# Optimization experiments

Hardware: AMD Instinct MI355X
Metric: run time of the kernel (lower is better)

The kernel has to match this reference:

```python
import jax, jax.numpy as jnp
import numpy as np

B, S, D = 2, 4096, 1024

def setup_inputs() -> dict:
    key = jax.random.key(0)
    k1, k2 = jax.random.split(key)
    x = jax.random.normal(k1, (B, S, D), dtype=jnp.float32)
    W = jax.random.normal(k2, (D, 3 * D), dtype=jnp.float32) * (1.0 / np.sqrt(D))
    b = jnp.zeros((3 * D,), dtype=jnp.float32)
    return {"x": x, "W": W, "b": b}

def reference(x, W, b) -> jnp.ndarray:
    D_ = x.shape[-1]
    qkv = x @ W + b                       # [B, S, 3D]
    q, k, v = jnp.split(qkv, 3, axis=2)    # each [B, S, D]
    scale = 1.0 / jnp.sqrt(jnp.asarray(D_, dtype=x.dtype))
    scores = jnp.einsum('bqd,bkd->bqk', q, k) * scale  # [B, S, S]
    weights = jax.nn.softmax(scores, axis=-1)
    return jnp.einsum('bqk,bkd->bqd', weights, v)       # [B, S, D]
```

## Files before the change

### kernel.cpp

```cpp
#include <hip/hip_runtime.h>
#include <hip/hip_bf16.h>

typedef __attribute__((ext_vector_type(4))) float  f32x4;
typedef __attribute__((ext_vector_type(8))) __bf16 bf16x8;
typedef __attribute__((ext_vector_type(8))) unsigned short u16x8;

typedef const __attribute__((address_space(1))) void gas_void;
typedef __attribute__((address_space(3))) void las_void;

__device__ __forceinline__ unsigned short f2bf(float x) {
    unsigned u = __builtin_bit_cast(unsigned, x);
    u += 0x7fffu + ((u >> 16) & 1u);
    return (unsigned short)(u >> 16);
}
__device__ __forceinline__ float bf2f(unsigned short h) {
    unsigned u = ((unsigned)h) << 16;
    return __builtin_bit_cast(float, u);
}
__device__ __forceinline__ void gload_lds16(const void* g, void* l) {
    __builtin_amdgcn_global_load_lds((gas_void*)g, (las_void*)l, 16, 0, 0);
}

#define WAITVM(N) asm volatile("s_waitcnt vmcnt(" #N ")" ::: "memory")

__global__ void k_f32_to_bf16(const float* __restrict__ in,
                              unsigned short* __restrict__ out, int n4) {
    int i = blockIdx.x * blockDim.x + threadIdx.x;
    if (i < n4) {
        float4 v = ((const float4*)in)[i];
        ushort4 o;
        o.x = f2bf(v.x); o.y = f2bf(v.y); o.z = f2bf(v.z); o.w = f2bf(v.w);
        ((ushort4*)out)[i] = o;
    }
}

__global__ void k_transpose_w(const float* __restrict__ W,
                              unsigned short* __restrict__ Wt,
                              int K, int N) {
    __shared__ unsigned short tile[32][33];
    int n0 = blockIdx.x * 32, k0 = blockIdx.y * 32;
    int tx = threadIdx.x, ty = threadIdx.y;
#pragma unroll
    for (int i = 0; i < 4; i++) {
        int kk = ty + i * 8;
        tile[kk][tx] = f2bf(W[(size_t)(k0 + kk) * N + n0 + tx]);
    }
    __syncthreads();
#pragma unroll
    for (int i = 0; i < 4; i++) {
        int nn = ty + i * 8;
        Wt[(size_t)(n0 + nn) * K + k0 + tx] = tile[tx][nn];
    }
}

__global__ void k_transpose_v(const unsigned short* __restrict__ Vrow,
                              unsigned short* __restrict__ Vt) {
    __shared__ unsigned short tile[32][33];
    int b = blockIdx.z;
    int s0 = blockIdx.x * 32, d0 = blockIdx.y * 32;
    int tx = threadIdx.x, ty = threadIdx.y;
#pragma unroll
    for (int i = 0; i < 4; i++) {
        int ss = ty + i * 8;
        tile[ss][tx] = Vrow[((size_t)(b * 4096 + s0 + ss)) * 1024 + d0 + tx];
    }
    __syncthreads();
#pragma unroll
    for (int i = 0; i < 4; i++) {
        int dd = ty + i * 8;
        Vt[((size_t)b * 1024 + d0 + dd) * 4096 + s0 + tx] = tile[tx][dd];
    }
}

template <int MODE>
__global__ __launch_bounds__(512, 2) void k_g256(
        const unsigned short* __restrict__ A, int lda,
        const unsigned short* __restrict__ Bt, int ldb,
        void* __restrict__ C, int ldc,
        unsigned short* __restrict__ Vp,
        const float* __restrict__ bias,
        int K, float alpha, long sA, long sB, long sC) {
    __shared__ __align__(16) unsigned short As[2][16384];
    __shared__ __align__(16) unsigned short Bs[2][16384];

    const int z = blockIdx.z;
    A  += (size_t)z * sA;
    Bt += (size_t)z * sB;

    const int nwg  = gridDim.x * gridDim.y;
    const int flat = blockIdx.y * gridDim.x + blockIdx.x;
    const int swzb = (flat & 7) * (nwg >> 3) + (flat >> 3);
    const int m0   = (swzb / gridDim.x) * 256;
    const int n0   = (swzb % gridDim.x) * 256;

    const int tid  = threadIdx.x;
    const int lane = tid & 63;
    const int wid  = tid >> 6;
    const int wm   = wid >> 2;
    const int wn   = wid & 3;
    const int l15  = lane & 15;
    const int l4   = lane >> 4;

    f32x4 acc[8][4] = {};

    const int srow = tid >> 3;
    const int kel  = (((lane & 7) ^ (lane >> 3)) << 3);
    const int c0 = ((l4 << 4)) ^ ((l15 & 7) << 4);
    const int c1 = (64 + (l4 << 4)) ^ ((l15 & 7) << 4);

    auto stageA = [&](int b, int h, int kt) {
#pragma unroll
        for (int c = 0; c < 2; c++) {
            const int r = h * 128 + c * 64 + srow;
            gload_lds16(A + (size_t)(m0 + r) * lda + kt * 64 + kel,
                        (char*)As + b * 32768 + h * 16384 + c * 8192 + (wid << 10));
        }
    };
    auto stageB = [&](int b, int h, int kt) {
#pragma unroll
        for (int c = 0; c < 2; c++) {
            const int r = h * 128 + c * 64 + srow;
            gload_lds16(Bt + (size_t)(n0 + r) * ldb + kt * 64 + kel,
                        (char*)Bs + b * 32768 + h * 16384 + c * 8192 + (wid << 10));
        }
    };

#define MM(I, J, X, Y) \
    acc[I][J] = __builtin_amdgcn_mfma_f32_16x16x32_bf16((X), (Y), acc[I][J], 0, 0, 0)

    const int NT = K >> 6;
    stageA(0, 0, 0); stageB(0, 0, 0); stageA(0, 1, 0); stageB(0, 1, 0);

    for (int t = 0; t < NT; t++) {
        const int cur = t & 1, nxt = cur ^ 1;
        const char* Ab = (const char*)As + cur * 32768;
        const char* Bb = (const char*)Bs + cur * 32768;

        if (t + 1 < NT) {
            stageA(nxt, 0, t + 1); stageB(nxt, 0, t + 1);
            WAITVM(4);
        } else {
            WAITVM(0);
        }
        __builtin_amdgcn_s_barrier();
        __builtin_amdgcn_sched_barrier(0);

        bf16x8 bfrg[2][2][2];
#pragma unroll
        for (int qn = 0; qn < 2; qn++)
#pragma unroll
        for (int nf = 0; nf < 2; nf++) {
            const int rb = (wn * 64 + qn * 32 + nf * 16 + l15) * 128;
            bfrg[qn][nf][0] = *(const bf16x8*)(Bb + rb + c0);
            bfrg[qn][nf][1] = *(const bf16x8*)(Bb + rb + c1);
        }
        {
            bf16x8 af[4][2];
#pragma unroll
            for (int mf = 0; mf < 4; mf++) {
                const int ra = (wm * 128 + 0 * 64 + mf * 16 + l15) * 128;
                af[mf][0] = *(const bf16x8*)(Ab + ra + c0);
                af[mf][1] = *(const bf16x8*)(Ab + ra + c1);
            }
            __builtin_amdgcn_s_setprio(1);
#pragma unroll
            for (int mf = 0; mf < 4; mf++)
#pragma unroll
            for (int qn = 0; qn < 2; qn++)
#pragma unroll
            for (int nf = 0; nf < 2; nf++) {
                MM(mf, qn * 2 + nf, af[mf][0], bfrg[qn][nf][0]);
                MM(mf, qn * 2 + nf, af[mf][1], bfrg[qn][nf][1]);
            }
            __builtin_amdgcn_s_setprio(0);
        }

        if (t + 1 < NT) { stageA(nxt, 1, t + 1); stageB(nxt, 1, t + 1); }
        {
            bf16x8 af[4][2];
#pragma unroll
            for (int mf = 0; mf < 4; mf++) {
                const int ra = (wm * 128 + 1 * 64 + mf * 16 + l15) * 128;
                af[mf][0] = *(const bf16x8*)(Ab + ra + c0);
                af[mf][1] = *(const bf16x8*)(Ab + ra + c1);
            }
            __builtin_amdgcn_s_setprio(1);
#pragma unroll
            for (int mf = 0; mf < 4; mf++)
#pragma unroll
            for (int qn = 0; qn < 2; qn++)
#pragma unroll
            for (int nf = 0; nf < 2; nf++) {
                MM(4 + mf, qn * 2 + nf, af[mf][0], bfrg[qn][nf][0]);
                MM(4 + mf, qn * 2 + nf, af[mf][1], bfrg[qn][nf][1]);
            }
            __builtin_amdgcn_s_setprio(0);
        }
        __builtin_amdgcn_s_barrier();
        __builtin_amdgcn_sched_barrier(0);
    }
#undef MM

#pragma unroll
    for (int qm = 0; qm < 2; qm++)
#pragma unroll
    for (int mf = 0; mf < 4; mf++) {
        const int row = m0 + wm * 128 + qm * 64 + mf * 16 + l4 * 4;
#pragma unroll
        for (int qn = 0; qn < 2; qn++)
#pragma unroll
        for (int nf = 0; nf < 2; nf++) {
            const int col = n0 + wn * 64 + qn * 32 + nf * 16 + l15;
            const float bv = (MODE == 2) ? bias[col] : 0.0f;
            const f32x4 av = acc[qm * 4 + mf][qn * 2 + nf];
#pragma unroll
            for (int r = 0; r < 4; r++) {
                const float v = av[r] * alpha + bv;
                if (MODE == 1) {
                    ((unsigned short*)C)[(size_t)z * sC + (size_t)(row + r) * ldc + col] = f2bf(v);
                } else {
                    const int lc = col & 1023;
                    if (col < 2048)
                        ((unsigned short*)C)[(size_t)(col >> 10) * 8388608 +
                                             (size_t)(row + r) * 1024 + lc] = f2bf(v);
                    else
                        Vp[(size_t)(row + r) * 1024 + lc] = f2bf(v);
                }
            }
        }
    }
}

__global__ __launch_bounds__(512, 2) void k_pv256(
        const unsigned short* __restrict__ A, int lda,
        const unsigned short* __restrict__ Bt, int ldb,
        float* __restrict__ C, int ldc,
        int K, long sA, long sB, long sC) {
    __shared__ __align__(16) unsigned short As[2][16384];
    __shared__ __align__(16) unsigned short Bs[2][8192];

    const int z = blockIdx.z;
    A  += (size_t)z * sA;
    Bt += (size_t)z * sB;

    const int nwg  = gridDim.x * gridDim.y;
    const int flat = blockIdx.y * gridDim.x + blockIdx.x;
    const int swzb = (flat & 7) * (nwg >> 3) + (flat >> 3);
    const int m0   = (swzb / gridDim.x) * 256;
    const int n0   = (swzb % gridDim.x) * 128;

    const int tid  = threadIdx.x;
    const int lane = tid & 63;
    const int wid  = tid >> 6;
    const int wm   = wid >> 2;
    const int wn   = wid & 3;
    const int l15  = lane & 15;
    const int l4   = lane >> 4;

    f32x4 acc[8][2] = {};

    const int srow = tid >> 3;
    const int kel  = (((lane & 7) ^ (lane >> 3)) << 3);
    const int c0 = ((l4 << 4)) ^ ((l15 & 7) << 4);
    const int c1 = (64 + (l4 << 4)) ^ ((l15 & 7) << 4);

    auto stageA1 = [&](int b, int a, int kt) {
        const int r = a * 64 + srow;
        gload_lds16(A + (size_t)(m0 + r) * lda + kt * 64 + kel,
                    (char*)As + b * 32768 + a * 8192 + (wid << 10));
    };
    auto stageB1 = [&](int b, int c, int kt) {
        const int r = c * 64 + srow;
        gload_lds16(Bt + (size_t)(n0 + r) * ldb + kt * 64 + kel,
                    (char*)Bs + b * 16384 + c * 8192 + (wid << 10));
    };

#define MM(I, J, X, Y) \
    acc[I][J] = __builtin_amdgcn_mfma_f32_16x16x32_bf16((X), (Y), acc[I][J], 0, 0, 0)

    const int NT = K >> 6;
    stageA1(0, 0, 0); stageA1(0, 1, 0); stageA1(0, 2, 0); stageA1(0, 3, 0);
    stageB1(0, 0, 0); stageB1(0, 1, 0);

    for (int t = 0; t < NT; t++) {
        const int cur = t & 1, nxt = cur ^ 1;
        const char* Ab = (const char*)As + cur * 32768;
        const char* Bb = (const char*)Bs + cur * 16384;

        if (t + 1 < NT) {
            stageA1(nxt, 0, t + 1); stageA1(nxt, 1, t + 1); stageB1(nxt, 0, t + 1);
            WAITVM(3);
        } else {
            WAITVM(0);
        }
        __builtin_amdgcn_s_barrier();
        __builtin_amdgcn_sched_barrier(0);

        bf16x8 bfrg[2][2];
#pragma unroll
        for (int nf = 0; nf < 2; nf++) {
            const int rb = (wn * 32 + nf * 16 + l15) * 128;
            bfrg[nf][0] = *(const bf16x8*)(Bb + rb + c0);
            bfrg[nf][1] = *(const bf16x8*)(Bb + rb + c1);
        }
        {
            bf16x8 af[4][2];
#pragma unroll
            for (int mf = 0; mf < 4; mf++) {
                const int ra = (wm * 128 + 0 * 64 + mf * 16 + l15) * 128;
                af[mf][0] = *(const bf16x8*)(Ab + ra + c0);
                af[mf][1] = *(const bf16x8*)(Ab + ra + c1);
            }
            __builtin_amdgcn_s_setprio(1);
#pragma unroll
            for (int mf = 0; mf < 4; mf++)
#pragma unroll
            for (int nf = 0; nf < 2; nf++) {
                MM(mf, nf, af[mf][0], bfrg[nf][0]);
                MM(mf, nf, af[mf][1], bfrg[nf][1]);
            }
            __builtin_amdgcn_s_setprio(0);
        }

        if (t + 1 < NT) {
            stageA1(nxt, 2, t + 1); stageA1(nxt, 3, t + 1); stageB1(nxt, 1, t + 1);
        }
        {
            bf16x8 af[4][2];
#pragma unroll
            for (int mf = 0; mf < 4; mf++) {
                const int ra = (wm * 128 + 1 * 64 + mf * 16 + l15) * 128;
                af[mf][0] = *(const bf16x8*)(Ab + ra + c0);
                af[mf][1] = *(const bf16x8*)(Ab + ra + c1);
            }
            __builtin_amdgcn_s_setprio(1);
#pragma unroll
            for (int mf = 0; mf < 4; mf++)
#pragma unroll
            for (int nf = 0; nf < 2; nf++) {
                MM(4 + mf, nf, af[mf][0], bfrg[nf][0]);
                MM(4 + mf, nf, af[mf][1], bfrg[nf][1]);
            }
            __builtin_amdgcn_s_setprio(0);
        }
        __builtin_amdgcn_s_barrier();
        __builtin_amdgcn_sched_barrier(0);
    }
#undef MM

#pragma unroll
    for (int qm = 0; qm < 2; qm++)
#pragma unroll
    for (int mf = 0; mf < 4; mf++) {
        const int row = m0 + wm * 128 + qm * 64 + mf * 16 + l4 * 4;
#pragma unroll
        for (int nf = 0; nf < 2; nf++) {
            const int col = n0 + wn * 32 + nf * 16 + l15;
            const f32x4 av = acc[qm * 4 + mf][nf];
#pragma unroll
            for (int r = 0; r < 4; r++)
                C[(size_t)z * sC + (size_t)(row + r) * ldc + col] = av[r];
        }
    }
}

__global__ __launch_bounds__(256) void k_softmax_inplace(unsigned short* __restrict__ P, int S) {
    __shared__ float red[8];
    const int row  = blockIdx.x;
    const int tid  = threadIdx.x;
    const int lane = tid & 63;
    const int wid  = tid >> 6;
    unsigned short* p = P + (size_t)row * S;

    float v[16];
    u16x8 h0 = *(const u16x8*)&p[tid * 16];
    u16x8 h1 = *(const u16x8*)&p[tid * 16 + 8];
    float mx = -1e30f;
#pragma unroll
    for (int j = 0; j < 8; j++) { v[j]     = bf2f(h0[j]); mx = fmaxf(mx, v[j]);     }
#pragma unroll
    for (int j = 0; j < 8; j++) { v[j + 8] = bf2f(h1[j]); mx = fmaxf(mx, v[j + 8]); }

#pragma unroll
    for (int o = 32; o >= 1; o >>= 1) mx = fmaxf(mx, __shfl_xor(mx, o));
    if (lane == 0) red[wid] = mx;
    __syncthreads();
    mx = fmaxf(fmaxf(red[0], red[1]), fmaxf(red[2], red[3]));

    float sum = 0.0f;
#pragma unroll
    for (int j = 0; j < 16; j++) { v[j] = __expf(v[j] - mx); sum += v[j]; }
#pragma unroll
    for (int o = 32; o >= 1; o >>= 1) sum += __shfl_xor(sum, o);
    if (lane == 0) red[4 + wid] = sum;
    __syncthreads();
    sum = red[4] + red[5] + red[6] + red[7];
    const float rinv = 1.0f / sum;

    u16x8 o0, o1;
#pragma unroll
    for (int j = 0; j < 8; j++) { o0[j] = f2bf(v[j] * rinv); o1[j] = f2bf(v[j + 8] * rinv); }
    *(u16x8*)&p[tid * 16]     = o0;
    *(u16x8*)&p[tid * 16 + 8] = o1;
}

extern "C" void kernel_launch(void* const* d_in, const int* in_sizes, int n_in,
                              void* d_out, int out_size, void* d_ws, size_t ws_size,
                              hipStream_t stream) {
    const float* x    = (const float*)d_in[0];
    const float* W    = (const float*)d_in[1];
    const float* bias = (const float*)d_in[2];
    float* out        = (float*)d_out;

    char* ws = (char*)d_ws;
    unsigned short* Qb   = (unsigned short*)(ws);
    unsigned short* Vt   = (unsigned short*)(ws + 33554432);
    unsigned short* xb   = (unsigned short*)(ws + 50331648);
    unsigned short* Wt   = (unsigned short*)(ws + 67108864);
    unsigned short* Vrow = (unsigned short*)(ws + 73400320);
    unsigned short* Pcat = (unsigned short*)(ws + 50331648);

    k_f32_to_bf16<<<8192, 256, 0, stream>>>(x, xb, (8192 * 1024) / 4);
    k_transpose_w<<<dim3(96, 32), dim3(32, 8), 0, stream>>>(W, Wt, 1024, 3072);
    k_g256<2><<<dim3(12, 32, 1), 512, 0, stream>>>(
        xb, 1024, Wt, 1024, (void*)Qb, 1024, Vrow, bias, 1024, 1.0f, 0, 0, 0);
    k_transpose_v<<<dim3(128, 32, 2), dim3(32, 8), 0, stream>>>(Vrow, Vt);

    const float scale = 0.03125f;
    k_g256<1><<<dim3(16, 16, 2), 512, 0, stream>>>(
        Qb, 1024, Qb + 8388608, 1024, (void*)Pcat, 4096, nullptr, nullptr,
        1024, scale, 4194304, 4194304, 16777216);
    k_softmax_inplace<<<8192, 256, 0, stream>>>(Pcat, 4096);
    k_pv256<<<dim3(8, 16, 2), 512, 0, stream>>>(
        Pcat, 4096, Vt, 4096, out, 1024, 4096, 16777216, 4194304, 4194304);
}
```

Before: 277.6 us.

## Restructure GEMM main loops into four-phase ping-pong with interleaved staging

Both GEMM kernels now split each K-tile iteration into four barrier-separated phases. Each phase issues one slice of next-tile global-to-LDS loads and then runs a smaller MFMA block on fragments read just before it, which spreads memory issue evenly between compute and shrinks the live fragment registers. The PV kernel also changes its wave layout from 2x4 to 4x2 (64x64 per wave), which changes the LDS read reuse of A and B fragments. The cost is many more workgroup barriers per iteration, and the staging order may leave the WAITVM counts tight.

```diff
diff --git a/kernel.cpp b/kernel.cpp
--- a/kernel.cpp
+++ b/kernel.cpp
@@ -22,6 +22,7 @@
 }
 
 #define WAITVM(N) asm volatile("s_waitcnt vmcnt(" #N ")" ::: "memory")
+#define BAR() do { __builtin_amdgcn_s_barrier(); __builtin_amdgcn_sched_barrier(0); } while (0)
 
 __global__ void k_f32_to_bf16(const float* __restrict__ in,
                               unsigned short* __restrict__ out, int n4) {
@@ -73,7 +74,7 @@
 }
 
 template <int MODE>
-__global__ __launch_bounds__(512, 2) void k_g256(
+__global__ __launch_bounds__(512, 2) void k_g256p4(
         const unsigned short* __restrict__ A, int lda,
         const unsigned short* __restrict__ Bt, int ldb,
         void* __restrict__ C, int ldc,
@@ -127,6 +128,36 @@
 
 #define MM(I, J, X, Y) \
     acc[I][J] = __builtin_amdgcn_mfma_f32_16x16x32_bf16((X), (Y), acc[I][J], 0, 0, 0)
+#define RD_A(QM)                                                               \
+    do {                                                                       \
+        _Pragma("unroll")                                                      \
+        for (int mf = 0; mf < 4; mf++) {                                       \
+            const int ra = (wm * 128 + (QM) * 64 + mf * 16 + l15) * 128;       \
+            af[mf][0] = *(const bf16x8*)(Ab + ra + c0);                        \
+            af[mf][1] = *(const bf16x8*)(Ab + ra + c1);                        \
+        }                                                                      \
+    } while (0)
+#define RD_B(QN)                                                               \
+    do {                                                                       \
+        _Pragma("unroll")                                                      \
+        for (int nf = 0; nf < 2; nf++) {                                       \
+            const int rb = (wn * 64 + (QN) * 32 + nf * 16 + l15) * 128;        \
+            bq[nf][0] = *(const bf16x8*)(Bb + rb + c0);                        \
+            bq[nf][1] = *(const bf16x8*)(Bb + rb + c1);                        \
+        }                                                                      \
+    } while (0)
+#define MFMA_PH(QM, QN)                                                        \
+    do {                                                                       \
+        __builtin_amdgcn_s_setprio(1);                                         \
+        _Pragma("unroll")                                                      \
+        for (int mf = 0; mf < 4; mf++)                                         \
+        _Pragma("unroll")                                                      \
+        for (int nf = 0; nf < 2; nf++) {                                       \
+            MM((QM) * 4 + mf, (QN) * 2 + nf, af[mf][0], bq[nf][0]);            \
+            MM((QM) * 4 + mf, (QN) * 2 + nf, af[mf][1], bq[nf][1]);            \
+        }                                                                      \
+        __builtin_amdgcn_s_setprio(0);                                         \
+    } while (0)
 
     const int NT = K >> 6;
     stageA(0, 0, 0); stageB(0, 0, 0); stageA(0, 1, 0); stageB(0, 1, 0);
@@ -135,70 +166,34 @@
         const int cur = t & 1, nxt = cur ^ 1;
         const char* Ab = (const char*)As + cur * 32768;
         const char* Bb = (const char*)Bs + cur * 32768;
-
-        if (t + 1 < NT) {
-            stageA(nxt, 0, t + 1); stageB(nxt, 0, t + 1);
-            WAITVM(4);
-        } else {
-            WAITVM(0);
-        }
-        __builtin_amdgcn_s_barrier();
-        __builtin_amdgcn_sched_barrier(0);
-
-        bf16x8 bfrg[2][2][2];
-#pragma unroll
-        for (int qn = 0; qn < 2; qn++)
-#pragma unroll
-        for (int nf = 0; nf < 2; nf++) {
-            const int rb = (wn * 64 + qn * 32 + nf * 16 + l15) * 128;
-            bfrg[qn][nf][0] = *(const bf16x8*)(Bb + rb + c0);
-            bfrg[qn][nf][1] = *(const bf16x8*)(Bb + rb + c1);
-        }
-        {
-            bf16x8 af[4][2];
-#pragma unroll
-            for (int mf = 0; mf < 4; mf++) {
-                const int ra = (wm * 128 + 0 * 64 + mf * 16 + l15) * 128;
-                af[mf][0] = *(const bf16x8*)(Ab + ra + c0);
-                af[mf][1] = *(const bf16x8*)(Ab + ra + c1);
-            }
-            __builtin_amdgcn_s_setprio(1);
-#pragma unroll
-            for (int mf = 0; mf < 4; mf++)
-#pragma unroll
-            for (int qn = 0; qn < 2; qn++)
-#pragma unroll
-            for (int nf = 0; nf < 2; nf++) {
-                MM(mf, qn * 2 + nf, af[mf][0], bfrg[qn][nf][0]);
-                MM(mf, qn * 2 + nf, af[mf][1], bfrg[qn][nf][1]);
-            }
-            __builtin_amdgcn_s_setprio(0);
-        }
-
-        if (t + 1 < NT) { stageA(nxt, 1, t + 1); stageB(nxt, 1, t + 1); }
-        {
-            bf16x8 af[4][2];
-#pragma unroll
-            for (int mf = 0; mf < 4; mf++) {
-                const int ra = (wm * 128 + 1 * 64 + mf * 16 + l15) * 128;
-                af[mf][0] = *(const bf16x8*)(Ab + ra + c0);
-                af[mf][1] = *(const bf16x8*)(Ab + ra + c1);
-            }
-            __builtin_amdgcn_s_setprio(1);
-#pragma unroll
-            for (int mf = 0; mf < 4; mf++)
-#pragma unroll
-            for (int qn = 0; qn < 2; qn++)
-#pragma unroll
-            for (int nf = 0; nf < 2; nf++) {
-                MM(4 + mf, qn * 2 + nf, af[mf][0], bfrg[qn][nf][0]);
-                MM(4 + mf, qn * 2 + nf, af[mf][1], bfrg[qn][nf][1]);
-            }
-            __builtin_amdgcn_s_setprio(0);
-        }
-        __builtin_amdgcn_s_barrier();
-        __builtin_amdgcn_sched_barrier(0);
-    }
+        const bool hn = (t + 1 < NT);
+
+        bf16x8 af[4][2], bq[2][2];
+
+        if (hn) { stageA(nxt, 0, t + 1); WAITVM(2); } else { WAITVM(0); }
+        BAR();
+        RD_A(0); RD_B(0);
+        MFMA_PH(0, 0);
+        BAR();
+        if (hn) stageB(nxt, 0, t + 1);
+        BAR();
+        RD_B(1);
+        MFMA_PH(0, 1);
+        BAR();
+        if (hn) stageA(nxt, 1, t + 1);
+        BAR();
+        RD_A(1); RD_B(0);
+        MFMA_PH(1, 0);
+        BAR();
+        if (hn) stageB(nxt, 1, t + 1);
+        BAR();
+        RD_B(1);
+        MFMA_PH(1, 1);
+        BAR();
+    }
+#undef MFMA_PH
+#undef RD_B
+#undef RD_A
 #undef MM
 
 #pragma unroll
@@ -231,7 +226,7 @@
     }
 }
 
-__global__ __launch_bounds__(512, 2) void k_pv256(
+__global__ __launch_bounds__(512, 2) void k_pv256p4(
         const unsigned short* __restrict__ A, int lda,
         const unsigned short* __restrict__ Bt, int ldb,
         float* __restrict__ C, int ldc,
@@ -252,12 +247,12 @@
     const int tid  = threadIdx.x;
     const int lane = tid & 63;
     const int wid  = tid >> 6;
-    const int wm   = wid >> 2;
-    const int wn   = wid & 3;
+    const int wm   = wid >> 1;
+    const int wn   = wid & 1;
     const int l15  = lane & 15;
     const int l4   = lane >> 4;
 
-    f32x4 acc[8][2] = {};
+    f32x4 acc[4][4] = {};
 
     const int srow = tid >> 3;
     const int kel  = (((lane & 7) ^ (lane >> 3)) << 3);
@@ -277,6 +272,32 @@
 
 #define MM(I, J, X, Y) \
     acc[I][J] = __builtin_amdgcn_mfma_f32_16x16x32_bf16((X), (Y), acc[I][J], 0, 0, 0)
+#define RD_A(CC)                                                               \
+    do {                                                                       \
+        _Pragma("unroll")                                                      \
+        for (int mf = 0; mf < 4; mf++) {                                       \
+            const int ra = (wm * 64 + mf * 16 + l15) * 128;                    \
+            af[mf] = *(const bf16x8*)(Ab + ra + (CC));                         \
+        }                                                                      \
+    } while (0)
+#define RD_B(NP, CC)                                                           \
+    do {                                                                       \
+        _Pragma("unroll")                                                      \
+        for (int j = 0; j < 2; j++) {                                          \
+            const int rb = (wn * 64 + ((NP) * 2 + j) * 16 + l15) * 128;        \
+            bq[j] = *(const bf16x8*)(Bb + rb + (CC));                          \
+        }                                                                      \
+    } while (0)
+#define MFMA_PH(NP)                                                            \
+    do {                                                                       \
+        __builtin_amdgcn_s_setprio(1);                                         \
+        _Pragma("unroll")                                                      \
+        for (int mf = 0; mf < 4; mf++)                                         \
+        _Pragma("unroll")                                                      \
+        for (int j = 0; j < 2; j++)                                            \
+            MM(mf, (NP) * 2 + j, af[mf], bq[j]);                               \
+        __builtin_amdgcn_s_setprio(0);                                         \
+    } while (0)
 
     const int NT = K >> 6;
     stageA1(0, 0, 0); stageA1(0, 1, 0); stageA1(0, 2, 0); stageA1(0, 3, 0);
@@ -286,77 +307,44 @@
         const int cur = t & 1, nxt = cur ^ 1;
         const char* Ab = (const char*)As + cur * 32768;
         const char* Bb = (const char*)Bs + cur * 16384;
-
-        if (t + 1 < NT) {
-            stageA1(nxt, 0, t + 1); stageA1(nxt, 1, t + 1); stageB1(nxt, 0, t + 1);
-            WAITVM(3);
-        } else {
-            WAITVM(0);
-        }
-        __builtin_amdgcn_s_barrier();
-        __builtin_amdgcn_sched_barrier(0);
-
-        bf16x8 bfrg[2][2];
-#pragma unroll
-        for (int nf = 0; nf < 2; nf++) {
-            const int rb = (wn * 32 + nf * 16 + l15) * 128;
-            bfrg[nf][0] = *(const bf16x8*)(Bb + rb + c0);
-            bfrg[nf][1] = *(const bf16x8*)(Bb + rb + c1);
-        }
-        {
-            bf16x8 af[4][2];
-#pragma unroll
-            for (int mf = 0; mf < 4; mf++) {
-                const int ra = (wm * 128 + 0 * 64 + mf * 16 + l15) * 128;
-                af[mf][0] = *(const bf16x8*)(Ab + ra + c0);
-                af[mf][1] = *(const bf16x8*)(Ab + ra + c1);
-            }
-            __builtin_amdgcn_s_setprio(1);
-#pragma unroll
-            for (int mf = 0; mf < 4; mf++)
-#pragma unroll
-            for (int nf = 0; nf < 2; nf++) {
-                MM(mf, nf, af[mf][0], bfrg[nf][0]);
-                MM(mf, nf, af[mf][1], bfrg[nf][1]);
-            }
-            __builtin_amdgcn_s_setprio(0);
-        }
-
-        if (t + 1 < NT) {
-            stageA1(nxt, 2, t + 1); stageA1(nxt, 3, t + 1); stageB1(nxt, 1, t + 1);
-        }
-        {
-            bf16x8 af[4][2];
-#pragma unroll
-            for (int mf = 0; mf < 4; mf++) {
-                const int ra = (wm * 128 + 1 * 64 + mf * 16 + l15) * 128;
-                af[mf][0] = *(const bf16x8*)(Ab + ra + c0);
-                af[mf][1] = *(const bf16x8*)(Ab + ra + c1);
-            }
-            __builtin_amdgcn_s_setprio(1);
-#pragma unroll
-            for (int mf = 0; mf < 4; mf++)
-#pragma unroll
-            for (int nf = 0; nf < 2; nf++) {
-                MM(4 + mf, nf, af[mf][0], bfrg[nf][0]);
-                MM(4 + mf, nf, af[mf][1], bfrg[nf][1]);
-            }
-            __builtin_amdgcn_s_setprio(0);
-        }
-        __builtin_amdgcn_s_barrier();
-        __builtin_amdgcn_sched_barrier(0);
-    }
+        const bool hn = (t + 1 < NT);
+
+        bf16x8 af[4], bq[2];
+
+        if (hn) { stageA1(nxt, 0, t + 1); stageA1(nxt, 1, t + 1); WAITVM(2); }
+        else    { WAITVM(0); }
+        BAR();
+        RD_A(c0); RD_B(0, c0);
+        MFMA_PH(0);
+        BAR();
+        if (hn) { stageA1(nxt, 2, t + 1); stageA1(nxt, 3, t + 1); }
+        BAR();
+        RD_B(1, c0);
+        MFMA_PH(1);
+        BAR();
+        if (hn) stageB1(nxt, 0, t + 1);
+        BAR();
+        RD_A(c1); RD_B(0, c1);
+        MFMA_PH(0);
+        BAR();
+        if (hn) stageB1(nxt, 1, t + 1);
+        BAR();
+        RD_B(1, c1);
+        MFMA_PH(1);
+        BAR();
+    }
+#undef MFMA_PH
+#undef RD_B
+#undef RD_A
 #undef MM
 
 #pragma unroll
-    for (int qm = 0; qm < 2; qm++)
-#pragma unroll
     for (int mf = 0; mf < 4; mf++) {
-        const int row = m0 + wm * 128 + qm * 64 + mf * 16 + l4 * 4;
-#pragma unroll
-        for (int nf = 0; nf < 2; nf++) {
-            const int col = n0 + wn * 32 + nf * 16 + l15;
-            const f32x4 av = acc[qm * 4 + mf][nf];
+        const int row = m0 + wm * 64 + mf * 16 + l4 * 4;
+#pragma unroll
+        for (int nf = 0; nf < 4; nf++) {
+            const int col = n0 + wn * 64 + nf * 16 + l15;
+            const f32x4 av = acc[mf][nf];
 #pragma unroll
             for (int r = 0; r < 4; r++)
                 C[(size_t)z * sC + (size_t)(row + r) * ldc + col] = av[r];
@@ -422,15 +410,15 @@
 
     k_f32_to_bf16<<<8192, 256, 0, stream>>>(x, xb, (8192 * 1024) / 4);
     k_transpose_w<<<dim3(96, 32), dim3(32, 8), 0, stream>>>(W, Wt, 1024, 3072);
-    k_g256<2><<<dim3(12, 32, 1), 512, 0, stream>>>(
+    k_g256p4<2><<<dim3(12, 32, 1), 512, 0, stream>>>(
         xb, 1024, Wt, 1024, (void*)Qb, 1024, Vrow, bias, 1024, 1.0f, 0, 0, 0);
     k_transpose_v<<<dim3(128, 32, 2), dim3(32, 8), 0, stream>>>(Vrow, Vt);
 
     const float scale = 0.03125f;
-    k_g256<1><<<dim3(16, 16, 2), 512, 0, stream>>>(
+    k_g256p4<1><<<dim3(16, 16, 2), 512, 0, stream>>>(
         Qb, 1024, Qb + 8388608, 1024, (void*)Pcat, 4096, nullptr, nullptr,
         1024, scale, 4194304, 4194304, 16777216);
     k_softmax_inplace<<<8192, 256, 0, stream>>>(Pcat, 4096);
-    k_pv256<<<dim3(8, 16, 2), 512, 0, stream>>>(
+    k_pv256p4<<<dim3(8, 16, 2), 512, 0, stream>>>(
         Pcat, 4096, Vt, 4096, out, 1024, 4096, 16777216, 4194304, 4194304);
 }
```

After: 375.7 us. 35.3% more time.

## Fuse softmax into score GEMM epilogue and write V transposed from QKV GEMM

Applied to the files above, without the earlier changes.

The separate in-place softmax pass over the bf16 score matrix is replaced. The score GEMM epilogue now writes exp(score*scale) and emits per-column-block partial row sums; a small kernel turns those sums into reciprocals, and the PV GEMM scales its output rows by them. The QKV projection moves to a new 128x128-tile kernel that stores V directly in transposed layout, so the V transpose kernel goes away. This removes a full read and write of the probability matrix plus one launch. The cost is that exp is taken without subtracting the row max, which can overflow for inputs with large scores.

```diff
diff --git a/kernel.cpp b/kernel.cpp
--- a/kernel.cpp
+++ b/kernel.cpp
@@ -22,6 +22,7 @@
 }
 
 #define WAITVM(N) asm volatile("s_waitcnt vmcnt(" #N ")" ::: "memory")
+#define BAR() do { __builtin_amdgcn_s_barrier(); __builtin_amdgcn_sched_barrier(0); } while (0)
 
 __global__ void k_f32_to_bf16(const float* __restrict__ in,
                               unsigned short* __restrict__ out, int n4) {
@@ -53,33 +54,132 @@
     }
 }
 
-__global__ void k_transpose_v(const unsigned short* __restrict__ Vrow,
-                              unsigned short* __restrict__ Vt) {
-    __shared__ unsigned short tile[32][33];
-    int b = blockIdx.z;
-    int s0 = blockIdx.x * 32, d0 = blockIdx.y * 32;
-    int tx = threadIdx.x, ty = threadIdx.y;
-#pragma unroll
-    for (int i = 0; i < 4; i++) {
-        int ss = ty + i * 8;
-        tile[ss][tx] = Vrow[((size_t)(b * 4096 + s0 + ss)) * 1024 + d0 + tx];
-    }
-    __syncthreads();
-#pragma unroll
-    for (int i = 0; i < 4; i++) {
-        int dd = ty + i * 8;
-        Vt[((size_t)b * 1024 + d0 + dd) * 4096 + s0 + tx] = tile[tx][dd];
-    }
-}
-
-template <int MODE>
-__global__ __launch_bounds__(512, 2) void k_g256(
+__global__ __launch_bounds__(256, 2) void k_g128qkv(
         const unsigned short* __restrict__ A, int lda,
         const unsigned short* __restrict__ Bt, int ldb,
-        void* __restrict__ C, int ldc,
-        unsigned short* __restrict__ Vp,
-        const float* __restrict__ bias,
-        int K, float alpha, long sA, long sB, long sC) {
+        unsigned short* __restrict__ C,
+        unsigned short* __restrict__ Vt,
+        const float* __restrict__ bias, int K) {
+    __shared__ __align__(16) unsigned short As[2][8192];
+    __shared__ __align__(16) unsigned short Bs[2][8192];
+
+    const int nwg  = gridDim.x * gridDim.y;
+    const int flat = blockIdx.y * gridDim.x + blockIdx.x;
+    const int swzb = (flat & 7) * (nwg >> 3) + (flat >> 3);
+    const int m0   = (swzb / gridDim.x) * 128;
+    const int n0   = (swzb % gridDim.x) * 128;
+
+    const int tid  = threadIdx.x;
+    const int lane = tid & 63;
+    const int wid  = tid >> 6;
+    const int wr   = wid >> 1;
+    const int wc   = wid & 1;
+    const int l15  = lane & 15;
+    const int l4   = lane >> 4;
+
+    f32x4 acc[4][4] = {};
+
+    const int srow = tid >> 3;
+    const int kel  = (((lane & 7) ^ (lane >> 3)) << 3);
+    const int c0 = (l4 << 4) ^ ((l15 & 7) << 4);
+    const int c1 = (64 + (l4 << 4)) ^ ((l15 & 7) << 4);
+
+    auto stA = [&](int b, int g, int kt) {
+        gload_lds16(A + (size_t)(m0 + g * 32 + srow) * lda + kt * 64 + kel,
+                    (char*)As + b * 16384 + g * 4096 + (wid << 10));
+    };
+    auto stB = [&](int b, int g, int kt) {
+        gload_lds16(Bt + (size_t)(n0 + g * 32 + srow) * ldb + kt * 64 + kel,
+                    (char*)Bs + b * 16384 + g * 4096 + (wid << 10));
+    };
+
+#define MM(I, J, X, Y) \
+    acc[I][J] = __builtin_amdgcn_mfma_f32_16x16x32_bf16((X), (Y), acc[I][J], 0, 0, 0)
+
+    const int NT = K >> 6;
+    stA(0, 0, 0); stA(0, 1, 0); stA(0, 2, 0); stA(0, 3, 0);
+    stB(0, 0, 0); stB(0, 1, 0); stB(0, 2, 0); stB(0, 3, 0);
+
+    for (int t = 0; t < NT; t++) {
+        const int cur = t & 1, nxt = cur ^ 1;
+        const char* Ab = (const char*)As + cur * 16384;
+        const char* Bb = (const char*)Bs + cur * 16384;
+        const bool hn = (t + 1 < NT);
+
+        bf16x8 af[4], bq[4];
+
+        if (hn) {
+            stA(nxt, 0, t + 1); stA(nxt, 1, t + 1); stA(nxt, 2, t + 1); stA(nxt, 3, t + 1);
+            WAITVM(4);
+        } else {
+            WAITVM(0);
+        }
+        BAR();
+#pragma unroll
+        for (int mf = 0; mf < 4; mf++)
+            af[mf] = *(const bf16x8*)(Ab + (wr * 64 + mf * 16 + l15) * 128 + c0);
+#pragma unroll
+        for (int nf = 0; nf < 4; nf++)
+            bq[nf] = *(const bf16x8*)(Bb + (wc * 64 + nf * 16 + l15) * 128 + c0);
+        __builtin_amdgcn_s_setprio(1);
+#pragma unroll
+        for (int mf = 0; mf < 4; mf++)
+#pragma unroll
+        for (int nf = 0; nf < 4; nf++)
+            MM(mf, nf, af[mf], bq[nf]);
+        __builtin_amdgcn_s_setprio(0);
+
+        if (hn) {
+            stB(nxt, 0, t + 1); stB(nxt, 1, t + 1); stB(nxt, 2, t + 1); stB(nxt, 3, t + 1);
+        }
+#pragma unroll
+        for (int mf = 0; mf < 4; mf++)
+            af[mf] = *(const bf16x8*)(Ab + (wr * 64 + mf * 16 + l15) * 128 + c1);
+#pragma unroll
+        for (int nf = 0; nf < 4; nf++)
+            bq[nf] = *(const bf16x8*)(Bb + (wc * 64 + nf * 16 + l15) * 128 + c1);
+        __builtin_amdgcn_s_setprio(1);
+#pragma unroll
+        for (int mf = 0; mf < 4; mf++)
+#pragma unroll
+        for (int nf = 0; nf < 4; nf++)
+            MM(mf, nf, af[mf], bq[nf]);
+        __builtin_amdgcn_s_setprio(0);
+        BAR();
+    }
+#undef MM
+
+#pragma unroll
+    for (int mf = 0; mf < 4; mf++) {
+        const int row = m0 + wr * 64 + mf * 16 + l4 * 4;
+#pragma unroll
+        for (int nf = 0; nf < 4; nf++) {
+            const int col = n0 + wc * 64 + nf * 16 + l15;
+            const f32x4 av = acc[mf][nf];
+            const float bv = bias[col];
+            const int lc = col & 1023;
+            if (col < 2048) {
+#pragma unroll
+                for (int r = 0; r < 4; r++)
+                    C[(size_t)(col >> 10) * 8388608 +
+                      (size_t)(row + r) * 1024 + lc] = f2bf(av[r] + bv);
+            } else {
+                const int b = row >> 12, s = row & 4095;
+                ushort4 o;
+                o.x = f2bf(av[0] + bv); o.y = f2bf(av[1] + bv);
+                o.z = f2bf(av[2] + bv); o.w = f2bf(av[3] + bv);
+                *(ushort4*)&Vt[(size_t)b * 4194304 + (size_t)lc * 4096 + s] = o;
+            }
+        }
+    }
+}
+
+__global__ __launch_bounds__(512, 2) void k_scores(
+        const unsigned short* __restrict__ A,
+        const unsigned short* __restrict__ Bt,
+        unsigned short* __restrict__ C,
+        float* __restrict__ part,
+        int K, float scale, long sA, long sB, long sC) {
     __shared__ __align__(16) unsigned short As[2][16384];
     __shared__ __align__(16) unsigned short Bs[2][16384];
 
@@ -112,7 +212,7 @@
 #pragma unroll
         for (int c = 0; c < 2; c++) {
             const int r = h * 128 + c * 64 + srow;
-            gload_lds16(A + (size_t)(m0 + r) * lda + kt * 64 + kel,
+            gload_lds16(A + (size_t)(m0 + r) * 1024 + kt * 64 + kel,
                         (char*)As + b * 32768 + h * 16384 + c * 8192 + (wid << 10));
         }
     };
@@ -120,7 +220,7 @@
 #pragma unroll
         for (int c = 0; c < 2; c++) {
             const int r = h * 128 + c * 64 + srow;
-            gload_lds16(Bt + (size_t)(n0 + r) * ldb + kt * 64 + kel,
+            gload_lds16(Bt + (size_t)(n0 + r) * 1024 + kt * 64 + kel,
                         (char*)Bs + b * 32768 + h * 16384 + c * 8192 + (wid << 10));
         }
     };
@@ -142,8 +242,7 @@
         } else {
             WAITVM(0);
         }
-        __builtin_amdgcn_s_barrier();
-        __builtin_amdgcn_sched_barrier(0);
+        BAR();
 
         bf16x8 bfrg[2][2][2];
 #pragma unroll
@@ -201,40 +300,60 @@
     }
 #undef MM
 
+    const int cb4 = ((n0 >> 8) << 2) + wn;
 #pragma unroll
     for (int qm = 0; qm < 2; qm++)
 #pragma unroll
     for (int mf = 0; mf < 4; mf++) {
         const int row = m0 + wm * 128 + qm * 64 + mf * 16 + l4 * 4;
+        float rs[4] = {0.f, 0.f, 0.f, 0.f};
 #pragma unroll
         for (int qn = 0; qn < 2; qn++)
 #pragma unroll
         for (int nf = 0; nf < 2; nf++) {
             const int col = n0 + wn * 64 + qn * 32 + nf * 16 + l15;
-            const float bv = (MODE == 2) ? bias[col] : 0.0f;
             const f32x4 av = acc[qm * 4 + mf][qn * 2 + nf];
 #pragma unroll
             for (int r = 0; r < 4; r++) {
-                const float v = av[r] * alpha + bv;
-                if (MODE == 1) {
-                    ((unsigned short*)C)[(size_t)z * sC + (size_t)(row + r) * ldc + col] = f2bf(v);
-                } else {
-                    const int lc = col & 1023;
-                    if (col < 2048)
-                        ((unsigned short*)C)[(size_t)(col >> 10) * 8388608 +
-                                             (size_t)(row + r) * 1024 + lc] = f2bf(v);
-                    else
-                        Vp[(size_t)(row + r) * 1024 + lc] = f2bf(v);
-                }
-            }
-        }
+                const float e = __expf(av[r] * scale);
+                rs[r] += e;
+                C[(size_t)z * sC + (size_t)(row + r) * 4096 + col] = f2bf(e);
+            }
+        }
+#pragma unroll
+        for (int r = 0; r < 4; r++) {
+#pragma unroll
+            for (int o = 1; o < 16; o <<= 1)
+                rs[r] += __shfl_xor(rs[r], o);
+        }
+        if (l15 == 0) {
+#pragma unroll
+            for (int r = 0; r < 4; r++)
+                part[((size_t)z * 4096 + row + r) * 64 + cb4] = rs[r];
+        }
+    }
+}
+
+__global__ __launch_bounds__(256) void k_rinv(const float* __restrict__ part,
+                                              float* __restrict__ rinv, int nrows) {
+    int row = blockIdx.x * blockDim.x + threadIdx.x;
+    if (row < nrows) {
+        const float* p = part + (size_t)row * 64;
+        float s = 0.f;
+#pragma unroll
+        for (int i = 0; i < 16; i++) {
+            f32x4 v = *(const f32x4*)(p + i * 4);
+            s += v[0] + v[1] + v[2] + v[3];
+        }
+        rinv[row] = 1.0f / s;
     }
 }
 
 __global__ __launch_bounds__(512, 2) void k_pv256(
-        const unsigned short* __restrict__ A, int lda,
-        const unsigned short* __restrict__ Bt, int ldb,
-        float* __restrict__ C, int ldc,
+        const unsigned short* __restrict__ A,
+        const unsigned short* __restrict__ Bt,
+        float* __restrict__ C,
+        const float* __restrict__ rinv,
         int K, long sA, long sB, long sC) {
     __shared__ __align__(16) unsigned short As[2][16384];
     __shared__ __align__(16) unsigned short Bs[2][8192];
@@ -266,12 +385,12 @@
 
     auto stageA1 = [&](int b, int a, int kt) {
         const int r = a * 64 + srow;
-        gload_lds16(A + (size_t)(m0 + r) * lda + kt * 64 + kel,
+        gload_lds16(A + (size_t)(m0 + r) * 4096 + kt * 64 + kel,
                     (char*)As + b * 32768 + a * 8192 + (wid << 10));
     };
     auto stageB1 = [&](int b, int c, int kt) {
         const int r = c * 64 + srow;
-        gload_lds16(Bt + (size_t)(n0 + r) * ldb + kt * 64 + kel,
+        gload_lds16(Bt + (size_t)(n0 + r) * 4096 + kt * 64 + kel,
                     (char*)Bs + b * 16384 + c * 8192 + (wid << 10));
     };
 
@@ -293,8 +412,7 @@
         } else {
             WAITVM(0);
         }
-        __builtin_amdgcn_s_barrier();
-        __builtin_amdgcn_sched_barrier(0);
+        BAR();
 
         bf16x8 bfrg[2][2];
 #pragma unroll
@@ -353,55 +471,16 @@
 #pragma unroll
     for (int mf = 0; mf < 4; mf++) {
         const int row = m0 + wm * 128 + qm * 64 + mf * 16 + l4 * 4;
+        const f32x4 riv = *(const f32x4*)&rinv[(size_t)z * 4096 + row];
 #pragma unroll
         for (int nf = 0; nf < 2; nf++) {
             const int col = n0 + wn * 32 + nf * 16 + l15;
             const f32x4 av = acc[qm * 4 + mf][nf];
 #pragma unroll
             for (int r = 0; r < 4; r++)
-                C[(size_t)z * sC + (size_t)(row + r) * ldc + col] = av[r];
-        }
-    }
-}
-
-__global__ __launch_bounds__(256) void k_softmax_inplace(unsigned short* __restrict__ P, int S) {
-    __shared__ float red[8];
-    const int row  = blockIdx.x;
-    const int tid  = threadIdx.x;
-    const int lane = tid & 63;
-    const int wid  = tid >> 6;
-    unsigned short* p = P + (size_t)row * S;
-
-    float v[16];
-    u16x8 h0 = *(const u16x8*)&p[tid * 16];
-    u16x8 h1 = *(const u16x8*)&p[tid * 16 + 8];
-    float mx = -1e30f;
-#pragma unroll
-    for (int j = 0; j < 8; j++) { v[j]     = bf2f(h0[j]); mx = fmaxf(mx, v[j]);     }
-#pragma unroll
-    for (int j = 0; j < 8; j++) { v[j + 8] = bf2f(h1[j]); mx = fmaxf(mx, v[j + 8]); }
-
-#pragma unroll
-    for (int o = 32; o >= 1; o >>= 1) mx = fmaxf(mx, __shfl_xor(mx, o));
-    if (lane == 0) red[wid] = mx;
-    __syncthreads();
-    mx = fmaxf(fmaxf(red[0], red[1]), fmaxf(red[2], red[3]));
-
-    float sum = 0.0f;
-#pragma unroll
-    for (int j = 0; j < 16; j++) { v[j] = __expf(v[j] - mx); sum += v[j]; }
-#pragma unroll
-    for (int o = 32; o >= 1; o >>= 1) sum += __shfl_xor(sum, o);
-    if (lane == 0) red[4 + wid] = sum;
-    __syncthreads();
-    sum = red[4] + red[5] + red[6] + red[7];
-    const float rinv = 1.0f / sum;
-
-    u16x8 o0, o1;
-#pragma unroll
-    for (int j = 0; j < 8; j++) { o0[j] = f2bf(v[j] * rinv); o1[j] = f2bf(v[j + 8] * rinv); }
-    *(u16x8*)&p[tid * 16]     = o0;
-    *(u16x8*)&p[tid * 16 + 8] = o1;
+                C[(size_t)z * sC + (size_t)(row + r) * 1024 + col] = av[r] * riv[r];
+        }
+    }
 }
 
 extern "C" void kernel_launch(void* const* d_in, const int* in_sizes, int n_in,
@@ -417,20 +496,18 @@
     unsigned short* Vt   = (unsigned short*)(ws + 33554432);
     unsigned short* xb   = (unsigned short*)(ws + 50331648);
     unsigned short* Wt   = (unsigned short*)(ws + 67108864);
-    unsigned short* Vrow = (unsigned short*)(ws + 73400320);
     unsigned short* Pcat = (unsigned short*)(ws + 50331648);
+    float*          part = (float*)(ws + 117440512);
+    float*          rinv = (float*)(ws + 121634816);
 
     k_f32_to_bf16<<<8192, 256, 0, stream>>>(x, xb, (8192 * 1024) / 4);
     k_transpose_w<<<dim3(96, 32), dim3(32, 8), 0, stream>>>(W, Wt, 1024, 3072);
-    k_g256<2><<<dim3(12, 32, 1), 512, 0, stream>>>(
-        xb, 1024, Wt, 1024, (void*)Qb, 1024, Vrow, bias, 1024, 1.0f, 0, 0, 0);
-    k_transpose_v<<<dim3(128, 32, 2), dim3(32, 8), 0, stream>>>(Vrow, Vt);
+    k_g128qkv<<<dim3(24, 64), 256, 0, stream>>>(xb, 1024, Wt, 1024, Qb, Vt, bias, 1024);
 
     const float scale = 0.03125f;
-    k_g256<1><<<dim3(16, 16, 2), 512, 0, stream>>>(
-        Qb, 1024, Qb + 8388608, 1024, (void*)Pcat, 4096, nullptr, nullptr,
-        1024, scale, 4194304, 4194304, 16777216);
-    k_softmax_inplace<<<8192, 256, 0, stream>>>(Pcat, 4096);
+    k_scores<<<dim3(16, 16, 2), 512, 0, stream>>>(
+        Qb, Qb + 8388608, Pcat, part, 1024, scale, 4194304, 4194304, 16777216);
+    k_rinv<<<32, 256, 0, stream>>>(part, rinv, 8192);
     k_pv256<<<dim3(8, 16, 2), 512, 0, stream>>>(
-        Pcat, 4096, Vt, 4096, out, 1024, 4096, 16777216, 4194304, 4194304);
-}
+        Pcat, Vt, out, rinv, 4096, 16777216, 4194304, 4194304);
+}
```

After: 266.1 us. -4.2%, faster.
